# Performance work log

Hardware: AMD Instinct MI355X
Metric: run time of the kernel (lower is better)

## Reference

```python
import jax, jax.numpy as jnp
import numpy as np

EPS = 1e-5


def gcn_conv(x, src, dst, n_nodes, W, b):
    # x: [B, N, Fin]; src/dst: [E+N] (self loops included); W: [Fout, Fin]
    h = jnp.einsum('bnf,of->bno', x, W)                      # [B, N, Fout]
    deg = jnp.zeros((n_nodes,), h.dtype).at[dst].add(1.0)    # in-degree of A+I
    dinv = jnp.where(deg > 0, 1.0 / jnp.sqrt(deg), 0.0)
    norm = dinv[src] * dinv[dst]                             # [E+N]
    msg = h[:, src, :] * norm[None, :, None]                 # gather along node axis
    out = jnp.zeros_like(h).at[:, dst, :].add(msg)           # scatter-add aggregate
    return out + b


def batchnorm_nodes(x, gamma, beta):
    # torch BatchNorm1d(N) on [B, N, C]: channel axis is N, stats over (B, C)
    mean = jnp.mean(x, axis=(0, 2), keepdims=True)
    var = jnp.mean(jnp.square(x - mean), axis=(0, 2), keepdims=True)
    xn = (x - mean) * jax.lax.rsqrt(var + EPS)
    return xn * gamma[None, :, None] + beta[None, :, None]


def setup_inputs() -> dict:
    key = jax.random.key(0)
    ks = jax.random.split(key, 20)
    B, N, FIN, D, OUT, E = 4096, 64, 67, 2048, 2, 512
    s = 0.1
    d = {}
    d['x_fingerprints'] = jax.random.normal(ks[0], (B, D), jnp.float32)
    d['x_node_features'] = jax.random.normal(ks[1], (B, N, FIN), jnp.float32)
    d['edge_list'] = jax.random.randint(ks[2], (2, E), 0, N)
    d['W1'] = jax.random.normal(ks[3], (64, FIN), jnp.float32) * s
    d['b1'] = jax.random.normal(ks[4], (64,), jnp.float32) * s
    d['g1'] = 1.0 + jax.random.normal(ks[5], (N,), jnp.float32) * s
    d['be1'] = jax.random.normal(ks[6], (N,), jnp.float32) * s
    d['W2'] = jax.random.normal(ks[7], (32, 64), jnp.float32) * s
    d['b2'] = jax.random.normal(ks[8], (32,), jnp.float32) * s
    d['g2'] = 1.0 + jax.random.normal(ks[9], (N,), jnp.float32) * s
    d['be2'] = jax.random.normal(ks[10], (N,), jnp.float32) * s
    d['Wl1'] = jax.random.normal(ks[11], (400, D), jnp.float32) * (s / 4)
    d['bl1'] = jax.random.normal(ks[12], (400,), jnp.float32) * s
    d['Wl2'] = jax.random.normal(ks[13], (64, 400), jnp.float32) * s
    d['bl2'] = jax.random.normal(ks[14], (64,), jnp.float32) * s
    d['Wfc'] = jax.random.normal(ks[15], (OUT, 96), jnp.float32) * s
    d['bfc'] = jax.random.normal(ks[16], (OUT,), jnp.float32) * s
    return d


def reference(x_fingerprints, x_node_features, edge_list, W1, b1, g1, be1,
              W2, b2, g2, be2, Wl1, bl1, Wl2, bl2, Wfc, bfc):
    B, N, _ = x_node_features.shape
    loops = jnp.arange(N)
    src = jnp.concatenate([edge_list[0], loops])  # add self loops (GCNConv default)
    dst = jnp.concatenate([edge_list[1], loops])
    g = gcn_conv(x_node_features, src, dst, N, W1, b1)
    g = jax.nn.relu(batchnorm_nodes(g, g1, be1))
    g = gcn_conv(g, src, dst, N, W2, b2)
    g = jax.nn.relu(batchnorm_nodes(g, g2, be2))           # [B, N, 32]
    pooled = jnp.max(g, axis=1)                             # global_max_pool -> [B, 32]
    h = jax.nn.relu(x_fingerprints @ Wl1.T + bl1)
    h = jax.nn.relu(h @ Wl2.T + bl2)                        # [B, 64]
    out = jnp.concatenate([pooled, h], axis=1) @ Wfc.T + bfc
    return out
```

## Files before the change

kernel.cpp:

```cpp
#include <hip/hip_runtime.h>
#include <hip/hip_bf16.h>
#include <math.h>

typedef __bf16 bf16;
typedef __attribute__((ext_vector_type(8))) __bf16 bf16x8;
typedef __attribute__((ext_vector_type(4))) __bf16 bf16x4;
typedef __attribute__((ext_vector_type(4))) float f32x4;

#define EPSBN 1e-5f
#define B_    4096
#define N_    64
#define FIN_  67
#define E_    512
#define TOT_E 576
#define NSLOT 128

__global__ __launch_bounds__(256) void k0_prep(const int* __restrict__ edge,
    float* __restrict__ partials,
    int* __restrict__ g_off, int* __restrict__ g_src, float* __restrict__ g_nrm)
{
    int tid = threadIdx.x;
    for (int i = blockIdx.x * 256 + tid; i < NSLOT * 64 * 4; i += gridDim.x * 256)
        partials[i] = 0.f;
    if (blockIdx.x != 0) return;

    __shared__ int ssrc[TOT_E], sdst[TOT_E];
    __shared__ int deg[N_], cnt[N_], off[N_ + 1];
    __shared__ float dinv[N_];
    for (int i = tid; i < TOT_E; i += 256) {
        int s, d;
        if (i < E_) { s = edge[i]; d = edge[E_ + i]; }
        else        { s = i - E_; d = i - E_; }
        ssrc[i] = s; sdst[i] = d;
    }
    if (tid < N_) { deg[tid] = 0; cnt[tid] = 0; }
    __syncthreads();
    for (int i = tid; i < TOT_E; i += 256) atomicAdd(&deg[sdst[i]], 1);
    __syncthreads();
    if (tid < N_) {
        dinv[tid] = rsqrtf((float)deg[tid]);
        int v = deg[tid];
        for (int o = 1; o < 64; o <<= 1) { int u = __shfl_up(v, o); if (tid >= o) v += u; }
        off[tid] = v - deg[tid];
        if (tid == 63) off[N_] = v;
    }
    __syncthreads();
    for (int i = tid; i < TOT_E; i += 256) {
        int d = sdst[i];
        int p = off[d] + atomicAdd(&cnt[d], 1);
        g_src[p] = ssrc[i];
        g_nrm[p] = dinv[ssrc[i]] * dinv[d];
    }
    if (tid <= N_) g_off[tid] = off[tid];
}

__global__ __launch_bounds__(256) void k1_gcn1(
    const float* __restrict__ x,
    const float* __restrict__ W1,
    const float* __restrict__ b1,
    const int* __restrict__ g_off, const int* __restrict__ g_src,
    const float* __restrict__ g_nrm,
    bf16* __restrict__ g1out,
    float* __restrict__ part1)
{
    __shared__ union {
        struct { bf16 xa[64 * 104]; bf16 wb[64 * 104]; } s0;
        struct { float hs[64 * 68]; } s1;
    } u;
    __shared__ int coff[N_ + 1];
    __shared__ int csrc[TOT_E];
    __shared__ float cnrm[TOT_E];

    int tid = threadIdx.x;
    int b = blockIdx.x;
    for (int i = tid; i <= N_; i += 256) coff[i] = g_off[i];
    for (int i = tid; i < TOT_E; i += 256) { csrc[i] = g_src[i]; cnrm[i] = g_nrm[i]; }

    const float* xb = x + (size_t)b * (N_ * FIN_);
    for (int i = tid; i < N_ * FIN_; i += 256) {
        int n = i / FIN_, f = i % FIN_;
        u.s0.xa[n * 104 + f] = (bf16)xb[i];
    }
    for (int i = tid; i < N_ * FIN_; i += 256) {
        int n = i / FIN_, f = i % FIN_;
        u.s0.wb[n * 104 + f] = (bf16)W1[i];
    }
    for (int i = tid; i < 64 * 29; i += 256) {
        int n = i / 29, f = 67 + i % 29;
        u.s0.xa[n * 104 + f] = (bf16)0.f;
        u.s0.wb[n * 104 + f] = (bf16)0.f;
    }
    __syncthreads();

    int w = tid >> 6, lane = tid & 63, q = lane >> 4, r15 = lane & 15;
    f32x4 z4 = {0.f, 0.f, 0.f, 0.f};
    f32x4 acc[4] = {z4, z4, z4, z4};
    int arow = w * 16 + r15;
#pragma unroll
    for (int kt = 0; kt < 3; ++kt) {
        bf16x8 a = *(const bf16x8*)&u.s0.xa[arow * 104 + kt * 32 + q * 8];
#pragma unroll
        for (int nt = 0; nt < 4; ++nt) {
            bf16x8 bb = *(const bf16x8*)&u.s0.wb[(nt * 16 + r15) * 104 + kt * 32 + q * 8];
            acc[nt] = __builtin_amdgcn_mfma_f32_16x16x32_bf16(a, bb, acc[nt], 0, 0, 0);
        }
    }
    __syncthreads();
#pragma unroll
    for (int nt = 0; nt < 4; ++nt)
#pragma unroll
        for (int r = 0; r < 4; ++r)
            u.s1.hs[(w * 16 + q * 4 + r) * 68 + nt * 16 + r15] = acc[nt][r];
    __syncthreads();

    int n = tid >> 2, oq = tid & 3;
    float a2[16];
#pragma unroll
    for (int j = 0; j < 16; ++j) a2[j] = 0.f;
    int e0 = coff[n], e1 = coff[n + 1];
    for (int e = e0; e < e1; ++e) {
        int s = csrc[e]; float wg = cnrm[e];
        const f32x4* hp = (const f32x4*)&u.s1.hs[s * 68 + oq * 16];
#pragma unroll
        for (int j4 = 0; j4 < 4; ++j4) {
            f32x4 hv = hp[j4];
            a2[j4 * 4 + 0] += wg * hv[0]; a2[j4 * 4 + 1] += wg * hv[1];
            a2[j4 * 4 + 2] += wg * hv[2]; a2[j4 * 4 + 3] += wg * hv[3];
        }
    }
    const f32x4* bp = (const f32x4*)&b1[oq * 16];
    float s1 = 0.f, s2 = 0.f;
    bf16x8 o0, o1;
#pragma unroll
    for (int j4 = 0; j4 < 4; ++j4) {
        f32x4 bv = bp[j4];
#pragma unroll
        for (int k = 0; k < 4; ++k) {
            float v = a2[j4 * 4 + k] + bv[k];
            s1 += v; s2 += v * v;
            if (j4 < 2) o0[j4 * 4 + k] = (bf16)v; else o1[(j4 - 2) * 4 + k] = (bf16)v;
        }
    }
    bf16* gp = g1out + ((size_t)b * 4096 + n * 64 + oq * 16);
    *(bf16x8*)gp = o0;
    *(bf16x8*)(gp + 8) = o1;
    s1 += __shfl_xor(s1, 1); s1 += __shfl_xor(s1, 2);
    s2 += __shfl_xor(s2, 1); s2 += __shfl_xor(s2, 2);
    if (oq == 0) {
        int slot = b & (NSLOT - 1);
        atomicAdd(&part1[(slot * 64 + n) * 2 + 0], s1);
        atomicAdd(&part1[(slot * 64 + n) * 2 + 1], s2);
    }
}

__global__ __launch_bounds__(64) void k_bnstats(
    const float* __restrict__ part,
    const float* __restrict__ gamma, const float* __restrict__ beta,
    float* __restrict__ scale, float* __restrict__ shift, float inv_count)
{
    int n = blockIdx.x, t = threadIdx.x;
    float s1 = part[(t * 64 + n) * 2] + part[((t + 64) * 64 + n) * 2];
    float s2 = part[(t * 64 + n) * 2 + 1] + part[((t + 64) * 64 + n) * 2 + 1];
#pragma unroll
    for (int o = 32; o > 0; o >>= 1) { s1 += __shfl_down(s1, o); s2 += __shfl_down(s2, o); }
    if (t == 0) {
        float mean = s1 * inv_count;
        float var = s2 * inv_count - mean * mean;
        float sc = gamma[n] * rsqrtf(var + EPSBN);
        scale[n] = sc;
        shift[n] = beta[n] - mean * sc;
    }
}

__global__ __launch_bounds__(256) void k3_gcn2(
    const bf16* __restrict__ g1out,
    const float* __restrict__ W2,
    const float* __restrict__ b2,
    const float* __restrict__ scale1, const float* __restrict__ shift1,
    const int* __restrict__ g_off, const int* __restrict__ g_src,
    const float* __restrict__ g_nrm,
    bf16* __restrict__ g2out,
    float* __restrict__ part2)
{
    __shared__ bf16 ya[64 * 72];
    __shared__ bf16 wb[32 * 72];
    __shared__ float hs[64 * 36];
    __shared__ int coff[N_ + 1];
    __shared__ int csrc[TOT_E];
    __shared__ float cnrm[TOT_E];
    __shared__ float ss1[64], sh1[64];

    int tid = threadIdx.x; int b = blockIdx.x;
    if (tid < 64) { ss1[tid] = scale1[tid]; sh1[tid] = shift1[tid]; }
    for (int i = tid; i <= N_; i += 256) coff[i] = g_off[i];
    for (int i = tid; i < TOT_E; i += 256) { csrc[i] = g_src[i]; cnrm[i] = g_nrm[i]; }
    for (int i = tid; i < 32 * 64; i += 256) {
        int o = i >> 6, f = i & 63;
        wb[o * 72 + f] = (bf16)W2[i];
    }
    __syncthreads();
    const bf16* gb = g1out + (size_t)b * 4096;
    for (int i = tid; i < 4096; i += 256) {
        int n = i >> 6;
        float v = (float)gb[i];
        float y = fmaxf(fmaf(ss1[n], v, sh1[n]), 0.f);
        ya[n * 72 + (i & 63)] = (bf16)y;
    }
    __syncthreads();

    int w = tid >> 6, lane = tid & 63, q = lane >> 4, r15 = lane & 15;
    f32x4 z4 = {0.f, 0.f, 0.f, 0.f};
    f32x4 acc[2] = {z4, z4};
#pragma unroll
    for (int kt = 0; kt < 2; ++kt) {
        bf16x8 a = *(const bf16x8*)&ya[(w * 16 + r15) * 72 + kt * 32 + q * 8];
#pragma unroll
        for (int nt = 0; nt < 2; ++nt) {
            bf16x8 bb = *(const bf16x8*)&wb[(nt * 16 + r15) * 72 + kt * 32 + q * 8];
            acc[nt] = __builtin_amdgcn_mfma_f32_16x16x32_bf16(a, bb, acc[nt], 0, 0, 0);
        }
    }
#pragma unroll
    for (int nt = 0; nt < 2; ++nt)
#pragma unroll
        for (int r = 0; r < 4; ++r)
            hs[(w * 16 + q * 4 + r) * 36 + nt * 16 + r15] = acc[nt][r];
    __syncthreads();

    int n = tid >> 2, oq = tid & 3;
    float a2[8] = {0, 0, 0, 0, 0, 0, 0, 0};
    int e0 = coff[n], e1 = coff[n + 1];
    for (int e = e0; e < e1; ++e) {
        int s = csrc[e]; float wg = cnrm[e];
        const f32x4* hp = (const f32x4*)&hs[s * 36 + oq * 8];
        f32x4 h0 = hp[0], h1v = hp[1];
        a2[0] += wg * h0[0]; a2[1] += wg * h0[1]; a2[2] += wg * h0[2]; a2[3] += wg * h0[3];
        a2[4] += wg * h1v[0]; a2[5] += wg * h1v[1]; a2[6] += wg * h1v[2]; a2[7] += wg * h1v[3];
    }
    const f32x4* bp = (const f32x4*)&b2[oq * 8];
    f32x4 b0 = bp[0], b1v = bp[1];
    float s1 = 0.f, s2 = 0.f; bf16x8 ov;
#pragma unroll
    for (int k = 0; k < 8; ++k) {
        float bias = (k < 4) ? b0[k] : b1v[k - 4];
        float v = a2[k] + bias;
        s1 += v; s2 += v * v;
        ov[k] = (bf16)v;
    }
    *(bf16x8*)(g2out + ((size_t)b * 2048 + n * 32 + oq * 8)) = ov;
    s1 += __shfl_xor(s1, 1); s1 += __shfl_xor(s1, 2);
    s2 += __shfl_xor(s2, 1); s2 += __shfl_xor(s2, 2);
    if (oq == 0) {
        int slot = b & (NSLOT - 1);
        atomicAdd(&part2[(slot * 64 + n) * 2 + 0], s1);
        atomicAdd(&part2[(slot * 64 + n) * 2 + 1], s2);
    }
}

__global__ __launch_bounds__(256) void k6_mlp1(
    const float* __restrict__ A,
    const float* __restrict__ Bw,
    float* __restrict__ part)
{
    __shared__ bf16 As[64 * 36];
    __shared__ bf16 Bs[64 * 36];
    int tid = threadIdx.x;
    int m0 = blockIdx.x * 64, n0 = blockIdx.y * 64, ks = blockIdx.z;
    int row = tid >> 2, seg = tid & 3;
    int w = tid >> 6, lane = tid & 63, q = lane >> 4, r15 = lane & 15;
    f32x4 z4 = {0.f, 0.f, 0.f, 0.f};
    f32x4 acc[4] = {z4, z4, z4, z4};
    const float* pA = A + (size_t)(m0 + row) * 2048 + ks * 512 + seg * 8;
    bool bvalid = (n0 + row) < 400;
    const float* pB = Bw + (size_t)(n0 + row) * 2048 + ks * 512 + seg * 8;

    f32x4 a0 = *(const f32x4*)pA;
    f32x4 a1 = *(const f32x4*)(pA + 4);
    f32x4 c0 = z4, c1 = z4;
    if (bvalid) { c0 = *(const f32x4*)pB; c1 = *(const f32x4*)(pB + 4); }

    for (int kt = 0; kt < 16; ++kt) {
        bf16x8 apk, bpk;
        apk[0] = (bf16)a0[0]; apk[1] = (bf16)a0[1]; apk[2] = (bf16)a0[2]; apk[3] = (bf16)a0[3];
        apk[4] = (bf16)a1[0]; apk[5] = (bf16)a1[1]; apk[6] = (bf16)a1[2]; apk[7] = (bf16)a1[3];
        bpk[0] = (bf16)c0[0]; bpk[1] = (bf16)c0[1]; bpk[2] = (bf16)c0[2]; bpk[3] = (bf16)c0[3];
        bpk[4] = (bf16)c1[0]; bpk[5] = (bf16)c1[1]; bpk[6] = (bf16)c1[2]; bpk[7] = (bf16)c1[3];
        __syncthreads();
        *(bf16x8*)&As[row * 36 + seg * 8] = apk;
        *(bf16x8*)&Bs[row * 36 + seg * 8] = bpk;
        __syncthreads();
        if (kt < 15) {
            pA += 32; pB += 32;
            a0 = *(const f32x4*)pA; a1 = *(const f32x4*)(pA + 4);
            if (bvalid) { c0 = *(const f32x4*)pB; c1 = *(const f32x4*)(pB + 4); }
        }
        bf16x8 a = *(const bf16x8*)&As[(w * 16 + r15) * 36 + q * 8];
#pragma unroll
        for (int nt = 0; nt < 4; ++nt) {
            bf16x8 bb = *(const bf16x8*)&Bs[(nt * 16 + r15) * 36 + q * 8];
            acc[nt] = __builtin_amdgcn_mfma_f32_16x16x32_bf16(a, bb, acc[nt], 0, 0, 0);
        }
    }
    float* pp = part + (size_t)ks * 1638400;
#pragma unroll
    for (int nt = 0; nt < 4; ++nt)
#pragma unroll
        for (int r = 0; r < 4; ++r) {
            int mm = m0 + w * 16 + q * 4 + r;
            int nn = n0 + nt * 16 + r15;
            if (nn < 400) pp[(size_t)mm * 400 + nn] = acc[nt][r];
        }
}

__global__ __launch_bounds__(256) void k6_reduce(
    const float* __restrict__ part,
    const float* __restrict__ bias,
    bf16* __restrict__ h1)
{
    int i = blockIdx.x * 256 + threadIdx.x;
    const f32x4* p = (const f32x4*)part;
    f32x4 s0 = p[i], s1v = p[i + 409600], s2v = p[i + 819200], s3v = p[i + 1228800];
    int nn = (i * 4) % 400;
    f32x4 bv = *(const f32x4*)&bias[nn];
    bf16x4 ov;
    ov[0] = (bf16)fmaxf(s0[0] + s1v[0] + s2v[0] + s3v[0] + bv[0], 0.f);
    ov[1] = (bf16)fmaxf(s0[1] + s1v[1] + s2v[1] + s3v[1] + bv[1], 0.f);
    ov[2] = (bf16)fmaxf(s0[2] + s1v[2] + s2v[2] + s3v[2] + bv[2], 0.f);
    ov[3] = (bf16)fmaxf(s0[3] + s1v[3] + s2v[3] + s3v[3] + bv[3], 0.f);
    *(bf16x4*)&h1[i * 4] = ov;
}

__global__ __launch_bounds__(256) void k7_mlp2(
    const bf16* __restrict__ A,
    const float* __restrict__ Bw,
    const float* __restrict__ bias,
    float* __restrict__ Cout)
{
    __shared__ bf16 As[16 * 416];
    int tid = threadIdx.x;
    int m0 = blockIdx.x * 16;
    for (int i = tid; i < 16 * 50; i += 256) {
        int rr = i / 50, cc = (i % 50) * 8;
        *(bf16x8*)&As[rr * 416 + cc] = *(const bf16x8*)(A + (size_t)(m0 + rr) * 400 + cc);
    }
    if (tid < 32) {
        int rr = tid >> 1, cc = 400 + (tid & 1) * 8;
        bf16x8 z;
#pragma unroll
        for (int k = 0; k < 8; ++k) z[k] = (bf16)0.f;
        *(bf16x8*)&As[rr * 416 + cc] = z;
    }
    __syncthreads();

    int w = tid >> 6, lane = tid & 63, q = lane >> 4, r15 = lane & 15;
    f32x4 acc = {0.f, 0.f, 0.f, 0.f};
    const float* pB = Bw + (size_t)(w * 16 + r15) * 400;
#pragma unroll 4
    for (int kt = 0; kt < 13; ++kt) {
        int k0 = kt * 32 + q * 8;
        bf16x8 a = *(const bf16x8*)&As[r15 * 416 + k0];
        bf16x8 bb;
#pragma unroll
        for (int k = 0; k < 8; ++k) bb[k] = (bf16)0.f;
        if (k0 < 400) {
            f32x4 c0 = *(const f32x4*)(pB + k0);
            f32x4 c1 = *(const f32x4*)(pB + k0 + 4);
            bb[0] = (bf16)c0[0]; bb[1] = (bf16)c0[1]; bb[2] = (bf16)c0[2]; bb[3] = (bf16)c0[3];
            bb[4] = (bf16)c1[0]; bb[5] = (bf16)c1[1]; bb[6] = (bf16)c1[2]; bb[7] = (bf16)c1[3];
        }
        acc = __builtin_amdgcn_mfma_f32_16x16x32_bf16(a, bb, acc, 0, 0, 0);
    }
#pragma unroll
    for (int r = 0; r < 4; ++r) {
        int mm = m0 + q * 4 + r;
        int nn = w * 16 + r15;
        float v = fmaxf(acc[r] + bias[nn], 0.f);
        Cout[(size_t)mm * 64 + nn] = v;
    }
}

__global__ __launch_bounds__(256) void k8_final(
    const bf16* __restrict__ g2out,
    const float* __restrict__ scale2, const float* __restrict__ shift2,
    const float* __restrict__ h2,
    const float* __restrict__ Wfc,
    const float* __restrict__ bfc,
    float* __restrict__ out)
{
    __shared__ float s2s[64], sh2s[64];
    int tid = threadIdx.x;
    if (tid < 64) { s2s[tid] = scale2[tid]; sh2s[tid] = shift2[tid]; }
    __syncthreads();
    int w = tid >> 6, lane = tid & 63;
    int b = blockIdx.x * 4 + w;
    int c = lane & 31, half = lane >> 5;
    const bf16* gb = g2out + (size_t)b * 2048;
    float mx = 0.f;
    for (int i = 0; i < 32; ++i) {
        int n = half * 32 + i;
        float v = (float)gb[n * 32 + c];
        float val = fmaf(s2s[n], v, sh2s[n]);
        mx = fmaxf(mx, val);
    }
    mx = fmaxf(mx, __shfl_xor(mx, 32));
    float h2v = h2[(size_t)b * 64 + lane];
#pragma unroll
    for (int o = 0; o < 2; ++o) {
        float t = h2v * Wfc[o * 96 + 32 + lane];
        if (half == 0) t += mx * Wfc[o * 96 + c];
#pragma unroll
        for (int off = 32; off > 0; off >>= 1) t += __shfl_xor(t, off);
        if (lane == 0) out[(size_t)b * 2 + o] = t + bfc[o];
    }
}

extern "C" void kernel_launch(void* const* d_in, const int* in_sizes, int n_in,
                              void* d_out, int out_size, void* d_ws, size_t ws_size,
                              hipStream_t stream)
{
    const float* x_fp   = (const float*)d_in[0];
    const float* x_node = (const float*)d_in[1];
    const int*   edge   = (const int*)d_in[2];
    const float* W1     = (const float*)d_in[3];
    const float* b1     = (const float*)d_in[4];
    const float* g1     = (const float*)d_in[5];
    const float* be1    = (const float*)d_in[6];
    const float* W2     = (const float*)d_in[7];
    const float* b2     = (const float*)d_in[8];
    const float* g2     = (const float*)d_in[9];
    const float* be2    = (const float*)d_in[10];
    const float* Wl1    = (const float*)d_in[11];
    const float* bl1    = (const float*)d_in[12];
    const float* Wl2    = (const float*)d_in[13];
    const float* bl2    = (const float*)d_in[14];
    const float* Wfc    = (const float*)d_in[15];
    const float* bfc    = (const float*)d_in[16];
    float* out = (float*)d_out;

    char* ws = (char*)d_ws;
    int*   csr_off = (int*)(ws);
    int*   csr_src = (int*)(ws + 512);
    float* csr_nrm = (float*)(ws + 3072);
    float* scale1  = (float*)(ws + 5632);
    float* shift1  = (float*)(ws + 5888);
    float* scale2  = (float*)(ws + 6144);
    float* shift2  = (float*)(ws + 6400);
    float* part1   = (float*)(ws + 8192);
    float* part2   = (float*)(ws + 8192 + 65536);
    bf16*  g1out   = (bf16*)(ws + 139264);
    float* part6   = (float*)(ws + 139264);
    bf16*  g2out   = (bf16*)(ws + 33693696ull);
    bf16*  h1      = (bf16*)(ws + 50470912ull);
    float* h2      = (float*)(ws + 53747712ull);

    k0_prep<<<dim3(64), dim3(256), 0, stream>>>(edge, part1, csr_off, csr_src, csr_nrm);
    k1_gcn1<<<dim3(4096), dim3(256), 0, stream>>>(x_node, W1, b1, csr_off, csr_src, csr_nrm,
                                                  g1out, part1);
    k_bnstats<<<dim3(64), dim3(64), 0, stream>>>(part1, g1, be1, scale1, shift1,
                                                 1.f / (4096.f * 64.f));
    k3_gcn2<<<dim3(4096), dim3(256), 0, stream>>>(g1out, W2, b2, scale1, shift1,
                                                  csr_off, csr_src, csr_nrm, g2out, part2);
    k_bnstats<<<dim3(64), dim3(64), 0, stream>>>(part2, g2, be2, scale2, shift2,
                                                 1.f / (4096.f * 32.f));
    k6_mlp1<<<dim3(64, 7, 4), dim3(256), 0, stream>>>(x_fp, Wl1, part6);
    k6_reduce<<<dim3(1600), dim3(256), 0, stream>>>(part6, bl1, h1);
    k7_mlp2<<<dim3(256), dim3(256), 0, stream>>>(h1, Wl2, bl2, h2);
    k8_final<<<dim3(1024), dim3(256), 0, stream>>>(g2out, scale2, shift2, h2, Wfc, bfc, out);
}
```

Baseline: 267.8 us.

## Replace CSR gather aggregation with dense normalized-adjacency MFMA using hi/lo bf16 split

Builds a dense 64x64 normalized adjacency matrix once in the prep kernel, stored as bf16 hi and lo parts. Both GCN kernels then do the neighbour aggregation as a matrix multiply on MFMA (three bf16 products, split for precision), replacing the per-node scalar gather loop over CSR edges. The prep kernel also pre-pads W1 and W2 to bf16 so each block can copy them with vector loads. Other changes: x is loaded raw and converted while the A fragments are built, BN1 is applied on the fly, and BN stats are reduced per row with shuffles. This trades scalar LDS gathers and per-block CSR/weight staging for extra MFMA work and some precision-compensation overhead.

```diff
diff --git a/kernel.cpp b/kernel.cpp
--- a/kernel.cpp
+++ b/kernel.cpp
@@ -12,145 +12,179 @@
 #define N_    64
 #define FIN_  67
 #define E_    512
-#define TOT_E 576
 #define NSLOT 128
 
 __global__ __launch_bounds__(256) void k0_prep(const int* __restrict__ edge,
+    const float* __restrict__ W1, const float* __restrict__ W2,
     float* __restrict__ partials,
-    int* __restrict__ g_off, int* __restrict__ g_src, float* __restrict__ g_nrm)
+    bf16* __restrict__ an_hi, bf16* __restrict__ an_lo,
+    bf16* __restrict__ wpad,
+    bf16* __restrict__ w2pad)
 {
     int tid = threadIdx.x;
     for (int i = blockIdx.x * 256 + tid; i < NSLOT * 64 * 4; i += gridDim.x * 256)
         partials[i] = 0.f;
+    if (blockIdx.x == 1) {
+        for (int i = tid; i < 64 * 104; i += 256) {
+            int n = i / 104, f = i % 104;
+            wpad[i] = (f < FIN_) ? (bf16)W1[n * FIN_ + f] : (bf16)0.f;
+        }
+        return;
+    }
+    if (blockIdx.x == 2) {
+        for (int i = tid; i < 32 * 72; i += 256) {
+            int o = i / 72, f = i % 72;
+            w2pad[i] = (f < 64) ? (bf16)W2[o * 64 + f] : (bf16)0.f;
+        }
+        return;
+    }
     if (blockIdx.x != 0) return;
 
-    __shared__ int ssrc[TOT_E], sdst[TOT_E];
-    __shared__ int deg[N_], cnt[N_], off[N_ + 1];
+    __shared__ float An[64 * 64];
+    __shared__ int ssrc[E_], sdst[E_];
+    __shared__ int deg[N_];
     __shared__ float dinv[N_];
-    for (int i = tid; i < TOT_E; i += 256) {
-        int s, d;
-        if (i < E_) { s = edge[i]; d = edge[E_ + i]; }
-        else        { s = i - E_; d = i - E_; }
-        ssrc[i] = s; sdst[i] = d;
-    }
-    if (tid < N_) { deg[tid] = 0; cnt[tid] = 0; }
-    __syncthreads();
-    for (int i = tid; i < TOT_E; i += 256) atomicAdd(&deg[sdst[i]], 1);
-    __syncthreads();
-    if (tid < N_) {
-        dinv[tid] = rsqrtf((float)deg[tid]);
-        int v = deg[tid];
-        for (int o = 1; o < 64; o <<= 1) { int u = __shfl_up(v, o); if (tid >= o) v += u; }
-        off[tid] = v - deg[tid];
-        if (tid == 63) off[N_] = v;
-    }
-    __syncthreads();
-    for (int i = tid; i < TOT_E; i += 256) {
-        int d = sdst[i];
-        int p = off[d] + atomicAdd(&cnt[d], 1);
-        g_src[p] = ssrc[i];
-        g_nrm[p] = dinv[ssrc[i]] * dinv[d];
-    }
-    if (tid <= N_) g_off[tid] = off[tid];
+    for (int i = tid; i < 64 * 64; i += 256) An[i] = 0.f;
+    for (int i = tid; i < E_; i += 256) { ssrc[i] = edge[i]; sdst[i] = edge[E_ + i]; }
+    if (tid < N_) deg[tid] = 1;
+    __syncthreads();
+    for (int i = tid; i < E_; i += 256) atomicAdd(&deg[sdst[i]], 1);
+    __syncthreads();
+    if (tid < N_) dinv[tid] = rsqrtf((float)deg[tid]);
+    __syncthreads();
+    for (int i = tid; i < E_; i += 256) {
+        int s = ssrc[i], d = sdst[i];
+        atomicAdd(&An[d * 64 + s], dinv[s] * dinv[d]);
+    }
+    if (tid < N_) atomicAdd(&An[tid * 64 + tid], dinv[tid] * dinv[tid]);
+    __syncthreads();
+    for (int i = tid; i < 64 * 64; i += 256) {
+        float v = An[i];
+        bf16 h = (bf16)v;
+        an_hi[i] = h;
+        an_lo[i] = (bf16)(v - (float)h);
+    }
 }
 
 __global__ __launch_bounds__(256) void k1_gcn1(
     const float* __restrict__ x,
-    const float* __restrict__ W1,
     const float* __restrict__ b1,
-    const int* __restrict__ g_off, const int* __restrict__ g_src,
-    const float* __restrict__ g_nrm,
+    const bf16* __restrict__ an_hi, const bf16* __restrict__ an_lo,
+    const bf16* __restrict__ wpad,
     bf16* __restrict__ g1out,
     float* __restrict__ part1)
 {
     __shared__ union {
-        struct { bf16 xa[64 * 104]; bf16 wb[64 * 104]; } s0;
-        struct { float hs[64 * 68]; } s1;
+        struct { float xraw[4352]; bf16 wb[64 * 104]; } s0;
+        struct { bf16 hhi[64 * 72]; bf16 hlo[64 * 72]; bf16 ost[64 * 72]; } s1;
     } u;
-    __shared__ int coff[N_ + 1];
-    __shared__ int csrc[TOT_E];
-    __shared__ float cnrm[TOT_E];
-
-    int tid = threadIdx.x;
-    int b = blockIdx.x;
-    for (int i = tid; i <= N_; i += 256) coff[i] = g_off[i];
-    for (int i = tid; i < TOT_E; i += 256) { csrc[i] = g_src[i]; cnrm[i] = g_nrm[i]; }
-
-    const float* xb = x + (size_t)b * (N_ * FIN_);
-    for (int i = tid; i < N_ * FIN_; i += 256) {
-        int n = i / FIN_, f = i % FIN_;
-        u.s0.xa[n * 104 + f] = (bf16)xb[i];
-    }
-    for (int i = tid; i < N_ * FIN_; i += 256) {
-        int n = i / FIN_, f = i % FIN_;
-        u.s0.wb[n * 104 + f] = (bf16)W1[i];
-    }
-    for (int i = tid; i < 64 * 29; i += 256) {
-        int n = i / 29, f = 67 + i % 29;
-        u.s0.xa[n * 104 + f] = (bf16)0.f;
-        u.s0.wb[n * 104 + f] = (bf16)0.f;
-    }
-    __syncthreads();
-
+    int tid = threadIdx.x, b = blockIdx.x;
     int w = tid >> 6, lane = tid & 63, q = lane >> 4, r15 = lane & 15;
+    int arow = w * 16 + r15;
+
+    const bf16* ahp = an_hi + arow * 64 + q * 8;
+    const bf16* alp = an_lo + arow * 64 + q * 8;
+    bf16x8 Ah0 = *(const bf16x8*)ahp;
+    bf16x8 Ah1 = *(const bf16x8*)(ahp + 32);
+    bf16x8 Al0 = *(const bf16x8*)alp;
+    bf16x8 Al1 = *(const bf16x8*)(alp + 32);
+
+    const f32x4* xb4 = (const f32x4*)(x + (size_t)b * (N_ * FIN_));
+    f32x4* xl4 = (f32x4*)u.s0.xraw;
+    for (int i = tid; i < 1072; i += 256) xl4[i] = xb4[i];
+    const bf16x8* wg8 = (const bf16x8*)wpad;
+    bf16x8* wl8 = (bf16x8*)u.s0.wb;
+    for (int i = tid; i < 832; i += 256) wl8[i] = wg8[i];
+    __syncthreads();
+
     f32x4 z4 = {0.f, 0.f, 0.f, 0.f};
     f32x4 acc[4] = {z4, z4, z4, z4};
-    int arow = w * 16 + r15;
+    const float* xr = u.s0.xraw + arow * FIN_;
 #pragma unroll
     for (int kt = 0; kt < 3; ++kt) {
-        bf16x8 a = *(const bf16x8*)&u.s0.xa[arow * 104 + kt * 32 + q * 8];
+        bf16x8 a;
+        int k0 = kt * 32 + q * 8;
+#pragma unroll
+        for (int j = 0; j < 8; ++j) {
+            int k = k0 + j;
+            a[j] = (k < FIN_) ? (bf16)xr[k] : (bf16)0.f;
+        }
 #pragma unroll
         for (int nt = 0; nt < 4; ++nt) {
-            bf16x8 bb = *(const bf16x8*)&u.s0.wb[(nt * 16 + r15) * 104 + kt * 32 + q * 8];
+            bf16x8 bb = *(const bf16x8*)&u.s0.wb[(nt * 16 + r15) * 104 + k0];
             acc[nt] = __builtin_amdgcn_mfma_f32_16x16x32_bf16(a, bb, acc[nt], 0, 0, 0);
         }
     }
     __syncthreads();
-#pragma unroll
-    for (int nt = 0; nt < 4; ++nt)
-#pragma unroll
-        for (int r = 0; r < 4; ++r)
-            u.s1.hs[(w * 16 + q * 4 + r) * 68 + nt * 16 + r15] = acc[nt][r];
-    __syncthreads();
-
+
+    int sbase = w * 16 + q * 4;
+#pragma unroll
+    for (int nt = 0; nt < 4; ++nt) {
+        int c = nt * 16 + r15;
+        bf16x4 hi, lo;
+#pragma unroll
+        for (int r = 0; r < 4; ++r) {
+            float v = acc[nt][r];
+            bf16 h = (bf16)v;
+            hi[r] = h;
+            lo[r] = (bf16)(v - (float)h);
+        }
+        *(bf16x4*)&u.s1.hhi[c * 72 + sbase] = hi;
+        *(bf16x4*)&u.s1.hlo[c * 72 + sbase] = lo;
+    }
+    __syncthreads();
+
+    f32x4 acc2[4] = {z4, z4, z4, z4};
+#pragma unroll
+    for (int kt = 0; kt < 2; ++kt) {
+        bf16x8 Ahk = kt ? Ah1 : Ah0;
+        bf16x8 Alk = kt ? Al1 : Al0;
+#pragma unroll
+        for (int nt = 0; nt < 4; ++nt) {
+            int o = (nt * 16 + r15) * 72 + kt * 32 + q * 8;
+            bf16x8 Hh = *(const bf16x8*)&u.s1.hhi[o];
+            bf16x8 Hl = *(const bf16x8*)&u.s1.hlo[o];
+            acc2[nt] = __builtin_amdgcn_mfma_f32_16x16x32_bf16(Ahk, Hh, acc2[nt], 0, 0, 0);
+            acc2[nt] = __builtin_amdgcn_mfma_f32_16x16x32_bf16(Ahk, Hl, acc2[nt], 0, 0, 0);
+            acc2[nt] = __builtin_amdgcn_mfma_f32_16x16x32_bf16(Alk, Hh, acc2[nt], 0, 0, 0);
+        }
+    }
+
+    float rs1[4] = {0.f, 0.f, 0.f, 0.f}, rs2[4] = {0.f, 0.f, 0.f, 0.f};
+#pragma unroll
+    for (int nt = 0; nt < 4; ++nt) {
+        int c = nt * 16 + r15;
+        float bc = b1[c];
+#pragma unroll
+        for (int r = 0; r < 4; ++r) {
+            float v = acc2[nt][r] + bc;
+            rs1[r] += v; rs2[r] += v * v;
+            u.s1.ost[(w * 16 + q * 4 + r) * 72 + c] = (bf16)v;
+        }
+    }
+#pragma unroll
+    for (int r = 0; r < 4; ++r)
+#pragma unroll
+        for (int o = 1; o < 16; o <<= 1) {
+            rs1[r] += __shfl_xor(rs1[r], o);
+            rs2[r] += __shfl_xor(rs2[r], o);
+        }
+    if (r15 == 0) {
+        int slot = b & (NSLOT - 1);
+#pragma unroll
+        for (int r = 0; r < 4; ++r) {
+            int d = w * 16 + q * 4 + r;
+            atomicAdd(&part1[(slot * 64 + d) * 2 + 0], rs1[r]);
+            atomicAdd(&part1[(slot * 64 + d) * 2 + 1], rs2[r]);
+        }
+    }
+    __syncthreads();
     int n = tid >> 2, oq = tid & 3;
-    float a2[16];
-#pragma unroll
-    for (int j = 0; j < 16; ++j) a2[j] = 0.f;
-    int e0 = coff[n], e1 = coff[n + 1];
-    for (int e = e0; e < e1; ++e) {
-        int s = csrc[e]; float wg = cnrm[e];
-        const f32x4* hp = (const f32x4*)&u.s1.hs[s * 68 + oq * 16];
-#pragma unroll
-        for (int j4 = 0; j4 < 4; ++j4) {
-            f32x4 hv = hp[j4];
-            a2[j4 * 4 + 0] += wg * hv[0]; a2[j4 * 4 + 1] += wg * hv[1];
-            a2[j4 * 4 + 2] += wg * hv[2]; a2[j4 * 4 + 3] += wg * hv[3];
-        }
-    }
-    const f32x4* bp = (const f32x4*)&b1[oq * 16];
-    float s1 = 0.f, s2 = 0.f;
-    bf16x8 o0, o1;
-#pragma unroll
-    for (int j4 = 0; j4 < 4; ++j4) {
-        f32x4 bv = bp[j4];
-#pragma unroll
-        for (int k = 0; k < 4; ++k) {
-            float v = a2[j4 * 4 + k] + bv[k];
-            s1 += v; s2 += v * v;
-            if (j4 < 2) o0[j4 * 4 + k] = (bf16)v; else o1[(j4 - 2) * 4 + k] = (bf16)v;
-        }
-    }
+    bf16x8 o0 = *(const bf16x8*)&u.s1.ost[n * 72 + oq * 16];
+    bf16x8 o1 = *(const bf16x8*)&u.s1.ost[n * 72 + oq * 16 + 8];
     bf16* gp = g1out + ((size_t)b * 4096 + n * 64 + oq * 16);
     *(bf16x8*)gp = o0;
     *(bf16x8*)(gp + 8) = o1;
-    s1 += __shfl_xor(s1, 1); s1 += __shfl_xor(s1, 2);
-    s2 += __shfl_xor(s2, 1); s2 += __shfl_xor(s2, 2);
-    if (oq == 0) {
-        int slot = b & (NSLOT - 1);
-        atomicAdd(&part1[(slot * 64 + n) * 2 + 0], s1);
-        atomicAdd(&part1[(slot * 64 + n) * 2 + 1], s2);
-    }
 }
 
 __global__ __launch_bounds__(64) void k_bnstats(
@@ -174,87 +208,120 @@
 
 __global__ __launch_bounds__(256) void k3_gcn2(
     const bf16* __restrict__ g1out,
-    const float* __restrict__ W2,
     const float* __restrict__ b2,
     const float* __restrict__ scale1, const float* __restrict__ shift1,
-    const int* __restrict__ g_off, const int* __restrict__ g_src,
-    const float* __restrict__ g_nrm,
+    const bf16* __restrict__ an_hi, const bf16* __restrict__ an_lo,
+    const bf16* __restrict__ w2pad,
     bf16* __restrict__ g2out,
     float* __restrict__ part2)
 {
-    __shared__ bf16 ya[64 * 72];
-    __shared__ bf16 wb[32 * 72];
-    __shared__ float hs[64 * 36];
-    __shared__ int coff[N_ + 1];
-    __shared__ int csrc[TOT_E];
-    __shared__ float cnrm[TOT_E];
-    __shared__ float ss1[64], sh1[64];
-
-    int tid = threadIdx.x; int b = blockIdx.x;
-    if (tid < 64) { ss1[tid] = scale1[tid]; sh1[tid] = shift1[tid]; }
-    for (int i = tid; i <= N_; i += 256) coff[i] = g_off[i];
-    for (int i = tid; i < TOT_E; i += 256) { csrc[i] = g_src[i]; cnrm[i] = g_nrm[i]; }
-    for (int i = tid; i < 32 * 64; i += 256) {
-        int o = i >> 6, f = i & 63;
-        wb[o * 72 + f] = (bf16)W2[i];
-    }
-    __syncthreads();
-    const bf16* gb = g1out + (size_t)b * 4096;
-    for (int i = tid; i < 4096; i += 256) {
-        int n = i >> 6;
-        float v = (float)gb[i];
-        float y = fmaxf(fmaf(ss1[n], v, sh1[n]), 0.f);
-        ya[n * 72 + (i & 63)] = (bf16)y;
-    }
-    __syncthreads();
-
+    __shared__ union {
+        struct { bf16 graw[4096]; bf16 wb[32 * 72]; } s0;
+        struct { bf16 hhi[32 * 72]; bf16 hlo[32 * 72]; bf16 ost[64 * 40]; } s1;
+    } u;
+    int tid = threadIdx.x, b = blockIdx.x;
     int w = tid >> 6, lane = tid & 63, q = lane >> 4, r15 = lane & 15;
+    int arow = w * 16 + r15;
+
+    const bf16* ahp = an_hi + arow * 64 + q * 8;
+    const bf16* alp = an_lo + arow * 64 + q * 8;
+    bf16x8 Ah0 = *(const bf16x8*)ahp;
+    bf16x8 Ah1 = *(const bf16x8*)(ahp + 32);
+    bf16x8 Al0 = *(const bf16x8*)alp;
+    bf16x8 Al1 = *(const bf16x8*)(alp + 32);
+    float sc = scale1[arow], sh = shift1[arow];
+
+    const bf16x8* gg8 = (const bf16x8*)(g1out + (size_t)b * 4096);
+    bf16x8* gl8 = (bf16x8*)u.s0.graw;
+    for (int i = tid; i < 512; i += 256) gl8[i] = gg8[i];
+    const bf16x8* wg8 = (const bf16x8*)w2pad;
+    bf16x8* wl8 = (bf16x8*)u.s0.wb;
+    for (int i = tid; i < 288; i += 256) wl8[i] = wg8[i];
+    __syncthreads();
+
     f32x4 z4 = {0.f, 0.f, 0.f, 0.f};
     f32x4 acc[2] = {z4, z4};
 #pragma unroll
     for (int kt = 0; kt < 2; ++kt) {
-        bf16x8 a = *(const bf16x8*)&ya[(w * 16 + r15) * 72 + kt * 32 + q * 8];
+        int k0 = kt * 32 + q * 8;
+        bf16x8 raw = *(const bf16x8*)&u.s0.graw[arow * 64 + k0];
+        bf16x8 a;
+#pragma unroll
+        for (int j = 0; j < 8; ++j)
+            a[j] = (bf16)fmaxf(fmaf(sc, (float)raw[j], sh), 0.f);
 #pragma unroll
         for (int nt = 0; nt < 2; ++nt) {
-            bf16x8 bb = *(const bf16x8*)&wb[(nt * 16 + r15) * 72 + kt * 32 + q * 8];
+            bf16x8 bb = *(const bf16x8*)&u.s0.wb[(nt * 16 + r15) * 72 + k0];
             acc[nt] = __builtin_amdgcn_mfma_f32_16x16x32_bf16(a, bb, acc[nt], 0, 0, 0);
         }
     }
-#pragma unroll
-    for (int nt = 0; nt < 2; ++nt)
-#pragma unroll
-        for (int r = 0; r < 4; ++r)
-            hs[(w * 16 + q * 4 + r) * 36 + nt * 16 + r15] = acc[nt][r];
-    __syncthreads();
-
+    __syncthreads();
+
+    int sbase = w * 16 + q * 4;
+#pragma unroll
+    for (int nt = 0; nt < 2; ++nt) {
+        int c = nt * 16 + r15;
+        bf16x4 hi, lo;
+#pragma unroll
+        for (int r = 0; r < 4; ++r) {
+            float v = acc[nt][r];
+            bf16 h = (bf16)v;
+            hi[r] = h;
+            lo[r] = (bf16)(v - (float)h);
+        }
+        *(bf16x4*)&u.s1.hhi[c * 72 + sbase] = hi;
+        *(bf16x4*)&u.s1.hlo[c * 72 + sbase] = lo;
+    }
+    __syncthreads();
+
+    f32x4 acc2[2] = {z4, z4};
+#pragma unroll
+    for (int kt = 0; kt < 2; ++kt) {
+        bf16x8 Ahk = kt ? Ah1 : Ah0;
+        bf16x8 Alk = kt ? Al1 : Al0;
+#pragma unroll
+        for (int nt = 0; nt < 2; ++nt) {
+            int o = (nt * 16 + r15) * 72 + kt * 32 + q * 8;
+            bf16x8 Hh = *(const bf16x8*)&u.s1.hhi[o];
+            bf16x8 Hl = *(const bf16x8*)&u.s1.hlo[o];
+            acc2[nt] = __builtin_amdgcn_mfma_f32_16x16x32_bf16(Ahk, Hh, acc2[nt], 0, 0, 0);
+            acc2[nt] = __builtin_amdgcn_mfma_f32_16x16x32_bf16(Ahk, Hl, acc2[nt], 0, 0, 0);
+            acc2[nt] = __builtin_amdgcn_mfma_f32_16x16x32_bf16(Alk, Hh, acc2[nt], 0, 0, 0);
+        }
+    }
+
+    float rs1[4] = {0.f, 0.f, 0.f, 0.f}, rs2[4] = {0.f, 0.f, 0.f, 0.f};
+#pragma unroll
+    for (int nt = 0; nt < 2; ++nt) {
+        int c = nt * 16 + r15;
+        float bc = b2[c];
+#pragma unroll
+        for (int r = 0; r < 4; ++r) {
+            float v = acc2[nt][r] + bc;
+            rs1[r] += v; rs2[r] += v * v;
+            u.s1.ost[(w * 16 + q * 4 + r) * 40 + c] = (bf16)v;
+        }
+    }
+#pragma unroll
+    for (int r = 0; r < 4; ++r)
+#pragma unroll
+        for (int o = 1; o < 16; o <<= 1) {
+            rs1[r] += __shfl_xor(rs1[r], o);
+            rs2[r] += __shfl_xor(rs2[r], o);
+        }
+    if (r15 == 0) {
+        int slot = b & (NSLOT - 1);
+#pragma unroll
+        for (int r = 0; r < 4; ++r) {
+            int d = w * 16 + q * 4 + r;
+            atomicAdd(&part2[(slot * 64 + d) * 2 + 0], rs1[r]);
+            atomicAdd(&part2[(slot * 64 + d) * 2 + 1], rs2[r]);
+        }
+    }
+    __syncthreads();
     int n = tid >> 2, oq = tid & 3;
-    float a2[8] = {0, 0, 0, 0, 0, 0, 0, 0};
-    int e0 = coff[n], e1 = coff[n + 1];
-    for (int e = e0; e < e1; ++e) {
-        int s = csrc[e]; float wg = cnrm[e];
-        const f32x4* hp = (const f32x4*)&hs[s * 36 + oq * 8];
-        f32x4 h0 = hp[0], h1v = hp[1];
-        a2[0] += wg * h0[0]; a2[1] += wg * h0[1]; a2[2] += wg * h0[2]; a2[3] += wg * h0[3];
-        a2[4] += wg * h1v[0]; a2[5] += wg * h1v[1]; a2[6] += wg * h1v[2]; a2[7] += wg * h1v[3];
-    }
-    const f32x4* bp = (const f32x4*)&b2[oq * 8];
-    f32x4 b0 = bp[0], b1v = bp[1];
-    float s1 = 0.f, s2 = 0.f; bf16x8 ov;
-#pragma unroll
-    for (int k = 0; k < 8; ++k) {
-        float bias = (k < 4) ? b0[k] : b1v[k - 4];
-        float v = a2[k] + bias;
-        s1 += v; s2 += v * v;
-        ov[k] = (bf16)v;
-    }
+    bf16x8 ov = *(const bf16x8*)&u.s1.ost[n * 40 + oq * 8];
     *(bf16x8*)(g2out + ((size_t)b * 2048 + n * 32 + oq * 8)) = ov;
-    s1 += __shfl_xor(s1, 1); s1 += __shfl_xor(s1, 2);
-    s2 += __shfl_xor(s2, 1); s2 += __shfl_xor(s2, 2);
-    if (oq == 0) {
-        int slot = b & (NSLOT - 1);
-        atomicAdd(&part2[(slot * 64 + n) * 2 + 0], s1);
-        atomicAdd(&part2[(slot * 64 + n) * 2 + 1], s2);
-    }
 }
 
 __global__ __launch_bounds__(256) void k6_mlp1(
@@ -438,9 +505,6 @@
     float* out = (float*)d_out;
 
     char* ws = (char*)d_ws;
-    int*   csr_off = (int*)(ws);
-    int*   csr_src = (int*)(ws + 512);
-    float* csr_nrm = (float*)(ws + 3072);
     float* scale1  = (float*)(ws + 5632);
     float* shift1  = (float*)(ws + 5888);
     float* scale2  = (float*)(ws + 6144);
@@ -452,14 +516,17 @@
     bf16*  g2out   = (bf16*)(ws + 33693696ull);
     bf16*  h1      = (bf16*)(ws + 50470912ull);
     float* h2      = (float*)(ws + 53747712ull);
-
-    k0_prep<<<dim3(64), dim3(256), 0, stream>>>(edge, part1, csr_off, csr_src, csr_nrm);
-    k1_gcn1<<<dim3(4096), dim3(256), 0, stream>>>(x_node, W1, b1, csr_off, csr_src, csr_nrm,
-                                                  g1out, part1);
+    bf16*  an_hi   = (bf16*)(ws + 53747712ull);
+    bf16*  an_lo   = (bf16*)(ws + 53747712ull + 8192);
+    bf16*  wpad    = (bf16*)(ws + 53747712ull + 16384);
+    bf16*  w2pad   = (bf16*)(ws + 53747712ull + 32768);
+
+    k0_prep<<<dim3(64), dim3(256), 0, stream>>>(edge, W1, W2, part1, an_hi, an_lo, wpad, w2pad);
+    k1_gcn1<<<dim3(4096), dim3(256), 0, stream>>>(x_node, b1, an_hi, an_lo, wpad, g1out, part1);
     k_bnstats<<<dim3(64), dim3(64), 0, stream>>>(part1, g1, be1, scale1, shift1,
                                                  1.f / (4096.f * 64.f));
-    k3_gcn2<<<dim3(4096), dim3(256), 0, stream>>>(g1out, W2, b2, scale1, shift1,
-                                                  csr_off, csr_src, csr_nrm, g2out, part2);
+    k3_gcn2<<<dim3(4096), dim3(256), 0, stream>>>(g1out, b2, scale1, shift1,
+                                                  an_hi, an_lo, w2pad, g2out, part2);
     k_bnstats<<<dim3(64), dim3(64), 0, stream>>>(part2, g2, be2, scale2, shift2,
                                                  1.f / (4096.f * 32.f));
     k6_mlp1<<<dim3(64, 7, 4), dim3(256), 0, stream>>>(x_fp, Wl1, part6);
```

Result: no change. 269.0 us (+0.5%).
